# Kernel tuning notes

Hardware: AMD Instinct MI355X
Metric: run time of the kernel (lower is better)

## Reference

```python
import jax, jax.numpy as jnp
import numpy as np

# Dims chosen per init_kwargs / input_specs
N_STEPS = 4      # n_hop * 2 sequential propagation steps
N_HEADS = 4
N = 4096         # number of graph nodes
D = 64           # input_dim == hid_dim (features are replaced each hop)
KEEP_RATIO = 0.5
TEMP = 0.2
NEG = -9e15      # large negative used by torch.where masking
EPS = 1e-12      # F.normalize eps


def setup_inputs() -> dict:
    key = jax.random.key(0)
    k1, k2, k3 = jax.random.split(key, 3)
    features = jax.random.normal(k1, (N, D), jnp.float32)
    # adjacency per propagation step, entries in {0,1}
    adj_lst = jax.random.randint(k2, (N_STEPS, N, N), 0, 2, jnp.int32)
    # per-step, per-head projection weights (xavier-ish scale)
    Ws = jax.random.normal(k3, (N_STEPS, N_HEADS, D, D), jnp.float32) * (1.0 / np.sqrt(D))
    return {"features": features, "adj_lst": adj_lst, "Ws": Ws}


def _hop(features, adj, W):
    """One propagation step, all heads fused.
    features: [N, D], adj: [N, N] int, W: [H, D, D] -> returns [N, D]."""
    h = jnp.einsum('nd,hde->hne', features, W)                         # [H,N,D]
    hn = h / (jnp.linalg.norm(h, axis=-1, keepdims=True) + EPS)        # row-normalize
    sim = jnp.einsum('hne,hme->hnm', hn, hn) / TEMP                    # cosine sim [H,N,N]
    mask = adj > 0                                                     # [N,N]
    sim_masked = jnp.where(mask, sim, NEG)
    row_max = jnp.max(sim_masked, axis=-1, keepdims=True)              # [H,N,1]
    # SimRatio keep rule: keep neighbors whose sim >= keep_ratio * row max
    keep = mask & (sim >= KEEP_RATIO * row_max)
    att = jax.nn.softmax(jnp.where(keep, sim, NEG), axis=-1)           # [H,N,N]
    out = jax.nn.elu(jnp.einsum('hnm,hme->hne', att, h))               # [H,N,D]
    # torch.stack(..., dim=2).mean(dim=2) == mean over heads
    return jnp.mean(out, axis=0)


def reference(features, adj_lst, Ws):
    x = features
    for i in range(N_STEPS):  # small fixed structural loop over hops
        x = _hop(x, adj_lst[i], Ws[i])
    return x
```

## Files before the change

kernel.cpp:

```cpp
#include <hip/hip_runtime.h>
#include <hip/hip_bf16.h>

#define N 4096
#define D 64
#define NH 4
#define NSTEP 4
#define HSTRIDE 262144

typedef short bf16x8 __attribute__((ext_vector_type(8)));
typedef float f32x4 __attribute__((ext_vector_type(4)));
typedef __hip_bfloat16 bf16;
typedef unsigned long long u64;

static const size_t OFF_MASK = 0;
static const size_t OFF_FEAT = (size_t)8 << 20;
static const size_t OFF_HNHI = (size_t)9 << 20;
static const size_t OFF_HNLO = (size_t)11 << 20;
static const size_t OFF_HTHI = (size_t)13 << 20;
static const size_t OFF_HTLO = (size_t)15 << 20;
static const size_t OFF_HOUT = (size_t)17 << 20;
static const size_t OFF_CM   = (size_t)21 << 20;

__global__ void k_packadj(const int* __restrict__ adj, u64* __restrict__ mt) {
    int t = threadIdx.x;
    int lane = t & 63;
    int row = blockIdx.x * 16 + (t >> 6) * 4 + (lane >> 4);
    int sub = lane & 15;
    int w = sub & 3;
    int c4 = sub >> 2;
    const int* rowp = adj + (size_t)row * N + w * 1024 + c4 * 4;
    u64 m0 = 0, m1 = 0, m2 = 0, m3 = 0;
    for (int i = 0; i < 64; ++i) {
        int4 v = *(const int4*)(rowp + i * 16);
        u64 b = 1ull << i;
        if (v.x > 0) m0 |= b;
        if (v.y > 0) m1 |= b;
        if (v.z > 0) m2 |= b;
        if (v.w > 0) m3 |= b;
    }
    u64* out = mt + (size_t)row * 64;
    out[(c4 * 4 + 0) * 4 + w] = m0;
    out[(c4 * 4 + 1) * 4 + w] = m1;
    out[(c4 * 4 + 2) * 4 + w] = m2;
    out[(c4 * 4 + 3) * 4 + w] = m3;
}

__global__ void k_phase0(const float* __restrict__ X, const float* __restrict__ hprev,
                         int use_hout, const float* __restrict__ W,
                         bf16* __restrict__ hnf_hi, bf16* __restrict__ hnf_lo,
                         bf16* __restrict__ htf_hi, bf16* __restrict__ htf_lo,
                         float* __restrict__ colmean) {
    __shared__ float Xs[64][65];
    __shared__ float Wsh[64][64];
    __shared__ float hbuf[64][68];
    __shared__ float rnbuf[64];
    __shared__ float colsum[64];
    int head = blockIdx.y;
    int r0 = blockIdx.x * 64;
    int t = threadIdx.x;
    for (int i = 0; i < 16; ++i) {
        int idx = t + 256 * i;
        int r = idx >> 6, c = idx & 63;
        float xv;
        if (use_hout) {
            size_t o = (size_t)(r0 + r) * 64 + c;
            xv = 0.25f * (hprev[o] + hprev[o + N * 64] + hprev[o + 2 * N * 64] + hprev[o + 3 * N * 64]);
        } else {
            xv = X[(size_t)(r0 + r) * 64 + c];
        }
        Xs[r][c] = xv;
        Wsh[r][c] = W[(size_t)head * 4096 + idx];
    }
    if (t < 64) colsum[t] = 0.f;
    __syncthreads();
    int lane = t & 63, w = t >> 6;
    int lr = w * 16 + (lane >> 2);
    int e0 = (lane & 3) * 16;
    float acc[16];
#pragma unroll
    for (int j = 0; j < 16; ++j) acc[j] = 0.f;
    for (int d = 0; d < 64; ++d) {
        float xv = Xs[lr][d];
#pragma unroll
        for (int j = 0; j < 16; ++j) acc[j] = fmaf(xv, Wsh[d][e0 + j], acc[j]);
    }
    float ss = 0.f;
#pragma unroll
    for (int j = 0; j < 16; ++j) ss = fmaf(acc[j], acc[j], ss);
    ss += __shfl_xor(ss, 1, 64);
    ss += __shfl_xor(ss, 2, 64);
    float rn = 1.0f / (sqrtf(ss) + 1e-12f);
#pragma unroll
    for (int j = 0; j < 16; ++j) hbuf[lr][e0 + j] = acc[j];
    if ((lane & 3) == 0) rnbuf[lr] = rn;
#pragma unroll
    for (int j = 0; j < 16; ++j) {
        float v = acc[j];
        v += __shfl_xor(v, 4, 64);
        v += __shfl_xor(v, 8, 64);
        v += __shfl_xor(v, 16, 64);
        v += __shfl_xor(v, 32, 64);
        if ((lane >> 2) == 0) atomicAdd(&colsum[e0 + j], v);
    }
    __syncthreads();
    if (t < 64) atomicAdd(&colmean[head * 64 + t], colsum[t] * (1.0f / N));

    size_t hb = (size_t)head * HSTRIDE;
    size_t hnbase = hb + (size_t)r0 * 64;
    size_t htbase = hb + (size_t)blockIdx.x * 4096;
#pragma unroll
    for (int u = 0; u < 2; ++u) {
        int idx16 = t * 2 + u;
        {
            int lnn = idx16 & 15, q = (idx16 >> 4) & 3, half = (idx16 >> 6) & 1, ctl = idx16 >> 7;
            int row = ctl * 16 + lnn, d0 = half * 32 + q * 8;
            float rr = rnbuf[row];
            bf16x8 hi8, lo8;
#pragma unroll
            for (int j = 0; j < 8; ++j) {
                float hnv = hbuf[row][d0 + j] * rr;
                bf16 nhi = __float2bfloat16(hnv);
                bf16 nlo = __float2bfloat16(hnv - __bfloat162float(nhi));
                hi8[j] = *(short*)&nhi;
                lo8[j] = *(short*)&nlo;
            }
            *(bf16x8*)(hnf_hi + hnbase + (size_t)idx16 * 8) = hi8;
            *(bf16x8*)(hnf_lo + hnbase + (size_t)idx16 * 8) = lo8;
        }
        {
            int dln = idx16 & 15, qq = (idx16 >> 4) & 3, half = (idx16 >> 6) & 1, nt = idx16 >> 7;
            int d = nt * 16 + dln, cbase = half * 32 + qq * 8;
            bf16x8 hi8, lo8;
#pragma unroll
            for (int j = 0; j < 8; ++j) {
                float hv = hbuf[cbase + j][d];
                bf16 hhi = __float2bfloat16(hv);
                bf16 hlo = __float2bfloat16(hv - __bfloat162float(hhi));
                hi8[j] = *(short*)&hhi;
                lo8[j] = *(short*)&hlo;
            }
            *(bf16x8*)(htf_hi + htbase + (size_t)idx16 * 8) = hi8;
            *(bf16x8*)(htf_lo + htbase + (size_t)idx16 * 8) = lo8;
        }
    }
}

struct BFrag { bf16x8 h0, h1, l0, l1; };

__device__ __forceinline__ BFrag load_bfrag(const bf16* __restrict__ hfh,
                                            const bf16* __restrict__ hfl,
                                            int ct, int lane) {
    BFrag f;
    size_t base = (size_t)ct * 1024 + lane * 8;
    f.h0 = *(const bf16x8*)(hfh + base);
    f.h1 = *(const bf16x8*)(hfh + base + 512);
    f.l0 = *(const bf16x8*)(hfl + base);
    f.l1 = *(const bf16x8*)(hfl + base + 512);
    return f;
}

__device__ __forceinline__ f32x4 sim_mfma(const BFrag& b,
                                          bf16x8 a0h, bf16x8 a1h, bf16x8 a0l, bf16x8 a1l) {
    f32x4 s = {0.f, 0.f, 0.f, 0.f};
    s = __builtin_amdgcn_mfma_f32_16x16x32_bf16(a0h, b.h0, s, 0, 0, 0);
    s = __builtin_amdgcn_mfma_f32_16x16x32_bf16(a1h, b.h1, s, 0, 0, 0);
    s = __builtin_amdgcn_mfma_f32_16x16x32_bf16(a0l, b.h0, s, 0, 0, 0);
    s = __builtin_amdgcn_mfma_f32_16x16x32_bf16(a1l, b.h1, s, 0, 0, 0);
    s = __builtin_amdgcn_mfma_f32_16x16x32_bf16(a0h, b.l0, s, 0, 0, 0);
    s = __builtin_amdgcn_mfma_f32_16x16x32_bf16(a1h, b.l1, s, 0, 0, 0);
    return s;
}

__launch_bounds__(256, 3)
__global__ void k_attn(const bf16* __restrict__ hnf_hi, const bf16* __restrict__ hnf_lo,
                       const bf16* __restrict__ htf_hi, const bf16* __restrict__ htf_lo,
                       const u64* __restrict__ mt,
                       const float* __restrict__ colmean,
                       float* __restrict__ hout) {
    __shared__ bf16 Plds[4][2][16 * 36];
    __shared__ float maxb[4][32];
    __shared__ float lbuf[4][16];
    __shared__ float pvbuf[4][16][66];
    int bid = blockIdx.x;
    int head = (bid & 7) >> 1;
    int rw = (((bid >> 3) << 1) | (bid & 1)) * 32;
    int t = threadIdx.x;
    int w = t >> 6, lane = t & 63;
    int ln = lane & 15, quad = lane >> 4;
    const bf16* hfh = hnf_hi + (size_t)head * HSTRIDE;
    const bf16* hfl = hnf_lo + (size_t)head * HSTRIDE;
    bf16x8 ah0[2], ah1[2], al0[2], al1[2];
#pragma unroll
    for (int rt = 0; rt < 2; ++rt) {
        size_t base = (size_t)((rw >> 4) + rt) * 1024 + lane * 8;
        ah0[rt] = *(const bf16x8*)(hfh + base);
        ah1[rt] = *(const bf16x8*)(hfh + base + 512);
        al0[rt] = *(const bf16x8*)(hfl + base);
        al1[rt] = *(const bf16x8*)(hfl + base + 512);
    }
    u64 mreg[2][4];
#pragma unroll
    for (int rt = 0; rt < 2; ++rt)
#pragma unroll
        for (int r = 0; r < 4; ++r)
            mreg[rt][r] = mt[((size_t)(rw + rt * 16 + quad * 4 + r) * 16 + ln) * 4 + w];

    const float NEGINF = -__builtin_inff();
    float m4[2][4];
#pragma unroll
    for (int rt = 0; rt < 2; ++rt)
#pragma unroll
        for (int r = 0; r < 4; ++r) m4[rt][r] = NEGINF;
    int ct0 = w * 64;

    for (int fi = 0; fi < 32; ++fi) {
        BFrag bt[2];
#pragma unroll
        for (int tt = 0; tt < 2; ++tt) bt[tt] = load_bfrag(hfh, hfl, ct0 + fi * 2 + tt, lane);
#pragma unroll
        for (int tt = 0; tt < 2; ++tt) {
            int bi = fi * 2 + tt;
#pragma unroll
            for (int rt = 0; rt < 2; ++rt) {
                f32x4 s = sim_mfma(bt[tt], ah0[rt], ah1[rt], al0[rt], al1[rt]);
#pragma unroll
                for (int r = 0; r < 4; ++r) {
                    unsigned int bit = (unsigned int)(mreg[rt][r] >> bi) & 1u;
                    float v = bit ? s[r] : NEGINF;
                    m4[rt][r] = fmaxf(m4[rt][r], v);
                }
            }
        }
    }
#pragma unroll
    for (int rt = 0; rt < 2; ++rt)
#pragma unroll
        for (int r = 0; r < 4; ++r) {
            float v = m4[rt][r];
            v = fmaxf(v, __shfl_xor(v, 1, 64));
            v = fmaxf(v, __shfl_xor(v, 2, 64));
            v = fmaxf(v, __shfl_xor(v, 4, 64));
            v = fmaxf(v, __shfl_xor(v, 8, 64));
            if (ln == 0) maxb[w][rt * 16 + quad * 4 + r] = v;
        }
    __syncthreads();
#pragma unroll
    for (int rt = 0; rt < 2; ++rt)
#pragma unroll
        for (int r = 0; r < 4; ++r) {
            int row = rt * 16 + quad * 4 + r;
            m4[rt][r] = fmaxf(fmaxf(maxb[0][row], maxb[1][row]),
                              fmaxf(maxb[2][row], maxb[3][row]));
        }

    const bf16* tfh = htf_hi + (size_t)head * HSTRIDE;
    const bf16* tfl = htf_lo + (size_t)head * HSTRIDE;
    float l4[2][4];
    f32x4 pv[2][4];
#pragma unroll
    for (int rt = 0; rt < 2; ++rt)
#pragma unroll
        for (int r = 0; r < 4; ++r) {
            l4[rt][r] = 0.f;
            pv[rt][r] = (f32x4){0.f, 0.f, 0.f, 0.f};
        }
    bf16* P0 = &Plds[w][0][0];
    bf16* P1 = &Plds[w][1][0];
    for (int fi = 0; fi < 32; ++fi) {
        BFrag bt[2];
#pragma unroll
        for (int tt = 0; tt < 2; ++tt) bt[tt] = load_bfrag(hfh, hfl, ct0 + fi * 2 + tt, lane);
#pragma unroll
        for (int tt = 0; tt < 2; ++tt) {
            int bi = fi * 2 + tt;
#pragma unroll
            for (int rt = 0; rt < 2; ++rt) {
                f32x4 s = sim_mfma(bt[tt], ah0[rt], ah1[rt], al0[rt], al1[rt]);
                bf16* P = rt ? P1 : P0;
#pragma unroll
                for (int r = 0; r < 4; ++r) {
                    unsigned int bit = (unsigned int)(mreg[rt][r] >> bi) & 1u;
                    bool keep = bit && (s[r] >= 0.5f * m4[rt][r]);
                    float arg = keep ? 5.0f * (s[r] - m4[rt][r]) : NEGINF;
                    float p = __expf(arg);
                    bf16 pb = __float2bfloat16(p);
                    l4[rt][r] += __bfloat162float(pb);
                    P[(quad * 4 + r) * 36 + tt * 16 + ln] = pb;
                }
            }
        }
        __builtin_amdgcn_wave_barrier();
        bf16x8 pa0 = *(const bf16x8*)(P0 + ln * 36 + quad * 8);
        bf16x8 pa1 = *(const bf16x8*)(P1 + ln * 36 + quad * 8);
        int c0 = w * 1024 + fi * 32;
        int g = c0 >> 6, half = (c0 >> 5) & 1;
#pragma unroll
        for (int nt = 0; nt < 4; ++nt) {
            size_t base = (size_t)(g * 8 + nt * 2 + half) * 512 + lane * 8;
            bf16x8 bh = *(const bf16x8*)(tfh + base);
            bf16x8 bl = *(const bf16x8*)(tfl + base);
            pv[0][nt] = __builtin_amdgcn_mfma_f32_16x16x32_bf16(pa0, bh, pv[0][nt], 0, 0, 0);
            pv[0][nt] = __builtin_amdgcn_mfma_f32_16x16x32_bf16(pa0, bl, pv[0][nt], 0, 0, 0);
            pv[1][nt] = __builtin_amdgcn_mfma_f32_16x16x32_bf16(pa1, bh, pv[1][nt], 0, 0, 0);
            pv[1][nt] = __builtin_amdgcn_mfma_f32_16x16x32_bf16(pa1, bl, pv[1][nt], 0, 0, 0);
        }
        __builtin_amdgcn_wave_barrier();
    }

    for (int rt = 0; rt < 2; ++rt) {
#pragma unroll
        for (int r = 0; r < 4; ++r) {
            float v = l4[rt][r];
            v += __shfl_xor(v, 1, 64);
            v += __shfl_xor(v, 2, 64);
            v += __shfl_xor(v, 4, 64);
            v += __shfl_xor(v, 8, 64);
            if (ln == 0) lbuf[w][quad * 4 + r] = v;
        }
#pragma unroll
        for (int nt = 0; nt < 4; ++nt)
#pragma unroll
            for (int r = 0; r < 4; ++r)
                pvbuf[w][quad * 4 + r][nt * 16 + ln] = pv[rt][nt][r];
        __syncthreads();
        {
            int row = t >> 4;
            int c4 = (t & 15) * 4;
            float lsum = lbuf[0][row] + lbuf[1][row] + lbuf[2][row] + lbuf[3][row];
            float inv = (lsum > 0.f) ? 1.0f / lsum : 0.f;
            float4 o;
            float* op = &o.x;
#pragma unroll
            for (int i = 0; i < 4; ++i) {
                int col = c4 + i;
                float v = pvbuf[0][row][col] + pvbuf[1][row][col]
                        + pvbuf[2][row][col] + pvbuf[3][row][col];
                v = (lsum > 0.f) ? v * inv : colmean[head * 64 + col];
                op[i] = (v > 0.f) ? v : (__expf(v) - 1.0f);
            }
            *(float4*)(hout + ((size_t)head * N + rw + rt * 16 + row) * 64 + c4) = o;
        }
        __syncthreads();
    }
}

__global__ void k_combine(const float* __restrict__ hout, float* __restrict__ outp) {
    int i = blockIdx.x * 256 + threadIdx.x;
    float v = 0.25f * (hout[i] + hout[i + N * 64] + hout[i + 2 * N * 64] + hout[i + 3 * N * 64]);
    outp[i] = v;
}

extern "C" void kernel_launch(void* const* d_in, const int* in_sizes, int n_in,
                              void* d_out, int out_size, void* d_ws, size_t ws_size,
                              hipStream_t stream) {
    const float* features_in = (const float*)d_in[0];
    const int* adj = (const int*)d_in[1];
    const float* Ws = (const float*)d_in[2];
    char* ws = (char*)d_ws;
    u64* mt = (u64*)(ws + OFF_MASK);
    bf16* hnf_hi = (bf16*)(ws + OFF_HNHI);
    bf16* hnf_lo = (bf16*)(ws + OFF_HNLO);
    bf16* htf_hi = (bf16*)(ws + OFF_HTHI);
    bf16* htf_lo = (bf16*)(ws + OFF_HTLO);
    float* hout = (float*)(ws + OFF_HOUT);
    float* cm = (float*)(ws + OFF_CM);

    k_packadj<<<dim3(NSTEP * N / 16), dim3(256), 0, stream>>>(adj, mt);
    for (int s = 0; s < NSTEP; ++s) {
        hipMemsetAsync(cm, 0, NH * D * sizeof(float), stream);
        k_phase0<<<dim3(64, NH), dim3(256), 0, stream>>>(features_in, hout, (s != 0),
                                                         Ws + (size_t)s * NH * D * D,
                                                         hnf_hi, hnf_lo, htf_hi, htf_lo, cm);
        k_attn<<<dim3(N / 32 * NH), dim3(256), 0, stream>>>(hnf_hi, hnf_lo, htf_hi, htf_lo,
                                                            mt + (size_t)s * N * 64, cm, hout);
    }
    k_combine<<<dim3(N * D / 256), dim3(256), 0, stream>>>(hout, (float*)d_out);
}
```

Measured before the change: 881.1 us.

## Split attention kernel into separate row-max pass and softmax/PV pass

Splits the fused attention kernel into two launches. The first computes the masked row maxima and writes them to a workspace buffer. The second reads those maxima and does the keep-rule softmax and P·V accumulation. Each kernel gets its own launch bounds (4 and 2 blocks per CU), so the max pass can run at higher occupancy. The cost is an extra launch per step and a small global round-trip for the row maxima.

```diff
diff --git a/kernel.cpp b/kernel.cpp
--- a/kernel.cpp
+++ b/kernel.cpp
@@ -13,7 +13,7 @@
 typedef unsigned long long u64;
 
 static const size_t OFF_MASK = 0;
-static const size_t OFF_FEAT = (size_t)8 << 20;
+static const size_t OFF_RMAX = (size_t)8 << 20;
 static const size_t OFF_HNHI = (size_t)9 << 20;
 static const size_t OFF_HNLO = (size_t)11 << 20;
 static const size_t OFF_HTHI = (size_t)13 << 20;
@@ -171,14 +171,78 @@
     return s;
 }
 
-__launch_bounds__(256, 3)
-__global__ void k_attn(const bf16* __restrict__ hnf_hi, const bf16* __restrict__ hnf_lo,
-                       const bf16* __restrict__ htf_hi, const bf16* __restrict__ htf_lo,
-                       const u64* __restrict__ mt,
-                       const float* __restrict__ colmean,
-                       float* __restrict__ hout) {
+__launch_bounds__(256, 4)
+__global__ void k_attn_a(const bf16* __restrict__ hnf_hi, const bf16* __restrict__ hnf_lo,
+                         const u64* __restrict__ mt, float* __restrict__ rowmax) {
+    __shared__ float maxb[4][32];
+    int bid = blockIdx.x;
+    int head = (bid & 7) >> 1;
+    int rw = (((bid >> 3) << 1) | (bid & 1)) * 32;
+    int t = threadIdx.x;
+    int w = t >> 6, lane = t & 63;
+    int ln = lane & 15, quad = lane >> 4;
+    const bf16* hfh = hnf_hi + (size_t)head * HSTRIDE;
+    const bf16* hfl = hnf_lo + (size_t)head * HSTRIDE;
+    bf16x8 ah0[2], ah1[2], al0[2], al1[2];
+#pragma unroll
+    for (int rt = 0; rt < 2; ++rt) {
+        size_t base = (size_t)((rw >> 4) + rt) * 1024 + lane * 8;
+        ah0[rt] = *(const bf16x8*)(hfh + base);
+        ah1[rt] = *(const bf16x8*)(hfh + base + 512);
+        al0[rt] = *(const bf16x8*)(hfl + base);
+        al1[rt] = *(const bf16x8*)(hfl + base + 512);
+    }
+    u64 mreg[2][4];
+#pragma unroll
+    for (int rt = 0; rt < 2; ++rt)
+#pragma unroll
+        for (int r = 0; r < 4; ++r)
+            mreg[rt][r] = mt[((size_t)(rw + rt * 16 + quad * 4 + r) * 16 + ln) * 4 + w];
+
+    const float NEGINF = -__builtin_inff();
+    float m4[2][4];
+#pragma unroll
+    for (int rt = 0; rt < 2; ++rt)
+#pragma unroll
+        for (int r = 0; r < 4; ++r) m4[rt][r] = NEGINF;
+    int ct0 = w * 64;
+
+    for (int bi = 0; bi < 64; ++bi) {
+        BFrag bt = load_bfrag(hfh, hfl, ct0 + bi, lane);
+#pragma unroll
+        for (int rt = 0; rt < 2; ++rt) {
+            f32x4 s = sim_mfma(bt, ah0[rt], ah1[rt], al0[rt], al1[rt]);
+#pragma unroll
+            for (int r = 0; r < 4; ++r) {
+                unsigned int bit = (unsigned int)(mreg[rt][r] >> bi) & 1u;
+                float v = bit ? s[r] : NEGINF;
+                m4[rt][r] = fmaxf(m4[rt][r], v);
+            }
+        }
+    }
+#pragma unroll
+    for (int rt = 0; rt < 2; ++rt)
+#pragma unroll
+        for (int r = 0; r < 4; ++r) {
+            float v = m4[rt][r];
+            v = fmaxf(v, __shfl_xor(v, 1, 64));
+            v = fmaxf(v, __shfl_xor(v, 2, 64));
+            v = fmaxf(v, __shfl_xor(v, 4, 64));
+            v = fmaxf(v, __shfl_xor(v, 8, 64));
+            if (ln == 0) maxb[w][rt * 16 + quad * 4 + r] = v;
+        }
+    __syncthreads();
+    if (t < 32)
+        rowmax[(size_t)head * N + rw + t] =
+            fmaxf(fmaxf(maxb[0][t], maxb[1][t]), fmaxf(maxb[2][t], maxb[3][t]));
+}
+
+__launch_bounds__(256, 2)
+__global__ void k_attn_b(const bf16* __restrict__ hnf_hi, const bf16* __restrict__ hnf_lo,
+                         const bf16* __restrict__ htf_hi, const bf16* __restrict__ htf_lo,
+                         const u64* __restrict__ mt, const float* __restrict__ rowmax,
+                         const float* __restrict__ colmean, float* __restrict__ hout) {
     __shared__ bf16 Plds[4][2][16 * 36];
-    __shared__ float maxb[4][32];
     __shared__ float lbuf[4][16];
     __shared__ float pvbuf[4][16][66];
     int bid = blockIdx.x;
@@ -199,60 +263,18 @@
         al1[rt] = *(const bf16x8*)(hfl + base + 512);
     }
     u64 mreg[2][4];
+    float m4[2][4];
 #pragma unroll
     for (int rt = 0; rt < 2; ++rt)
 #pragma unroll
-        for (int r = 0; r < 4; ++r)
-            mreg[rt][r] = mt[((size_t)(rw + rt * 16 + quad * 4 + r) * 16 + ln) * 4 + w];
+        for (int r = 0; r < 4; ++r) {
+            int row = rw + rt * 16 + quad * 4 + r;
+            mreg[rt][r] = mt[((size_t)row * 16 + ln) * 4 + w];
+            m4[rt][r] = rowmax[(size_t)head * N + row];
+        }
 
     const float NEGINF = -__builtin_inff();
-    float m4[2][4];
-#pragma unroll
-    for (int rt = 0; rt < 2; ++rt)
-#pragma unroll
-        for (int r = 0; r < 4; ++r) m4[rt][r] = NEGINF;
     int ct0 = w * 64;
-
-    for (int fi = 0; fi < 32; ++fi) {
-        BFrag bt[2];
-#pragma unroll
-        for (int tt = 0; tt < 2; ++tt) bt[tt] = load_bfrag(hfh, hfl, ct0 + fi * 2 + tt, lane);
-#pragma unroll
-        for (int tt = 0; tt < 2; ++tt) {
-            int bi = fi * 2 + tt;
-#pragma unroll
-            for (int rt = 0; rt < 2; ++rt) {
-                f32x4 s = sim_mfma(bt[tt], ah0[rt], ah1[rt], al0[rt], al1[rt]);
-#pragma unroll
-                for (int r = 0; r < 4; ++r) {
-                    unsigned int bit = (unsigned int)(mreg[rt][r] >> bi) & 1u;
-                    float v = bit ? s[r] : NEGINF;
-                    m4[rt][r] = fmaxf(m4[rt][r], v);
-                }
-            }
-        }
-    }
-#pragma unroll
-    for (int rt = 0; rt < 2; ++rt)
-#pragma unroll
-        for (int r = 0; r < 4; ++r) {
-            float v = m4[rt][r];
-            v = fmaxf(v, __shfl_xor(v, 1, 64));
-            v = fmaxf(v, __shfl_xor(v, 2, 64));
-            v = fmaxf(v, __shfl_xor(v, 4, 64));
-            v = fmaxf(v, __shfl_xor(v, 8, 64));
-            if (ln == 0) maxb[w][rt * 16 + quad * 4 + r] = v;
-        }
-    __syncthreads();
-#pragma unroll
-    for (int rt = 0; rt < 2; ++rt)
-#pragma unroll
-        for (int r = 0; r < 4; ++r) {
-            int row = rt * 16 + quad * 4 + r;
-            m4[rt][r] = fmaxf(fmaxf(maxb[0][row], maxb[1][row]),
-                              fmaxf(maxb[2][row], maxb[3][row]));
-        }
-
     const bf16* tfh = htf_hi + (size_t)head * HSTRIDE;
     const bf16* tfl = htf_lo + (size_t)head * HSTRIDE;
     float l4[2][4];
@@ -358,6 +380,7 @@
     const float* Ws = (const float*)d_in[2];
     char* ws = (char*)d_ws;
     u64* mt = (u64*)(ws + OFF_MASK);
+    float* rowmax = (float*)(ws + OFF_RMAX);
     bf16* hnf_hi = (bf16*)(ws + OFF_HNHI);
     bf16* hnf_lo = (bf16*)(ws + OFF_HNLO);
     bf16* htf_hi = (bf16*)(ws + OFF_HTHI);
@@ -371,8 +394,11 @@
         k_phase0<<<dim3(64, NH), dim3(256), 0, stream>>>(features_in, hout, (s != 0),
                                                          Ws + (size_t)s * NH * D * D,
                                                          hnf_hi, hnf_lo, htf_hi, htf_lo, cm);
-        k_attn<<<dim3(N / 32 * NH), dim3(256), 0, stream>>>(hnf_hi, hnf_lo, htf_hi, htf_lo,
-                                                            mt + (size_t)s * N * 64, cm, hout);
+        k_attn_a<<<dim3(N / 32 * NH), dim3(256), 0, stream>>>(hnf_hi, hnf_lo,
+                                                              mt + (size_t)s * N * 64, rowmax);
+        k_attn_b<<<dim3(N / 32 * NH), dim3(256), 0, stream>>>(hnf_hi, hnf_lo, htf_hi, htf_lo,
+                                                              mt + (size_t)s * N * 64, rowmax,
+                                                              cm, hout);
     }
     k_combine<<<dim3(N * D / 256), dim3(256), 0, stream>>>(hout, (float*)d_out);
 }
```

After: 892.1 us. No clear change (+1.2%).
